# Kernel optimization log

Measured on AMD Instinct MI355X. Metric: run time of the kernel, lower is better.

The kernel has to match this reference:

```python
import jax, jax.numpy as jnp
import numpy as np

D_MODEL = 2048
NUM_HEADS = 16
HEAD_DIM = D_MODEL // NUM_HEADS
EPS = 1e-6


def setup_inputs() -> dict:
    key = jax.random.key(0)
    ks = jax.random.split(key, 5)
    B, S = 1, 4096
    scale = 1.0 / np.sqrt(D_MODEL)
    return {
        "x": jax.random.normal(ks[0], (B, S, D_MODEL), dtype=jnp.float32),
        "wq": jax.random.normal(ks[1], (D_MODEL, D_MODEL), dtype=jnp.float32) * scale,
        "wk": jax.random.normal(ks[2], (D_MODEL, D_MODEL), dtype=jnp.float32) * scale,
        "wv": jax.random.normal(ks[3], (D_MODEL, D_MODEL), dtype=jnp.float32) * scale,
        "wo": jax.random.normal(ks[4], (D_MODEL, D_MODEL), dtype=jnp.float32) * scale,
        "q_norm_w": jnp.ones((HEAD_DIM,), dtype=jnp.float32),
        "k_norm_w": jnp.ones((HEAD_DIM,), dtype=jnp.float32),
    }


def _rmsnorm(x, w):
    rms = jnp.sqrt(jnp.mean(x * x, axis=-1, keepdims=True) + EPS)
    return x / rms * w


def reference(x, wq, wk, wv, wo, q_norm_w, k_norm_w):
    B, S, _ = x.shape
    # nn.Linear: y = x @ W.T ; split heads -> [B, H, S, Dh]
    def proj(w):
        return (x @ w.T).reshape(B, S, NUM_HEADS, HEAD_DIM).transpose(0, 2, 1, 3)
    q = _rmsnorm(proj(wq), q_norm_w)
    k = _rmsnorm(proj(wk), k_norm_w)
    v = proj(wv)
    scale = 1.0 / np.sqrt(HEAD_DIM)
    attn = jnp.einsum("bhqd,bhkd->bhqk", q, k) * scale  # [B,H,S,S]
    attn = jax.nn.softmax(attn, axis=-1)
    out = jnp.einsum("bhqk,bhkd->bhqd", attn, v)
    out = out.transpose(0, 2, 1, 3).reshape(B, S, D_MODEL)
    return out @ wo.T
```

## Files before the change

kernel.cpp:

```cpp
#include <hip/hip_runtime.h>
#include <hip/hip_bf16.h>

#define S 4096
#define D 2048
#define NH 16
#define HD 128

typedef __attribute__((ext_vector_type(8))) short bf16x8;
typedef __attribute__((ext_vector_type(4))) float f32x4;

typedef __attribute__((address_space(1))) char glob_char;
typedef __attribute__((address_space(3))) char lds_char_t;

__device__ __forceinline__ void gld16(const void* g, void* l) {
    __builtin_amdgcn_global_load_lds((const glob_char*)g, (lds_char_t*)l, 16, 0, 0);
}

__device__ __forceinline__ unsigned short f2b(float f) {
    union { float f; unsigned u; } c; c.f = f;
    unsigned r = c.u + 0x7fff + ((c.u >> 16) & 1);
    return (unsigned short)(r >> 16);
}
__device__ __forceinline__ float b2f(unsigned short u) {
    union { unsigned u; float f; } c; c.u = ((unsigned)u) << 16;
    return c.f;
}

__device__ __forceinline__ float fexp2(float x) {
#if __has_builtin(__builtin_amdgcn_exp2f)
    return __builtin_amdgcn_exp2f(x);
#else
    return __expf(x * 0.6931471805599453f);
#endif
}

#define MFMA16(a, b, c) __builtin_amdgcn_mfma_f32_16x16x32_bf16((a), (b), (c), 0, 0, 0)

__global__ __launch_bounds__(256) void cvt_all(
    const float* __restrict__ x,  const float* __restrict__ wq,
    const float* __restrict__ wk, const float* __restrict__ wv,
    const float* __restrict__ wo,
    unsigned short* __restrict__ xb, unsigned short* __restrict__ wqkvb,
    unsigned short* __restrict__ wob)
{
    const int z = blockIdx.y;
    const float* src; unsigned short* dst; int n4;
    if (z == 0)      { src = x;  dst = xb;                        n4 = (S * D) / 4; }
    else if (z == 1) { src = wq; dst = wqkvb;                     n4 = (D * D) / 4; }
    else if (z == 2) { src = wk; dst = wqkvb + (size_t)D * D;     n4 = (D * D) / 4; }
    else if (z == 3) { src = wv; dst = wqkvb + 2 * (size_t)D * D; n4 = (D * D) / 4; }
    else             { src = wo; dst = wob;                       n4 = (D * D) / 4; }
    int i = blockIdx.x * 256 + threadIdx.x;
    if (i < n4) {
        float4 v = ((const float4*)src)[i];
        ushort4 o;
        o.x = f2b(v.x); o.y = f2b(v.y); o.z = f2b(v.z); o.w = f2b(v.w);
        ((ushort4*)dst)[i] = o;
    }
}

__global__ __launch_bounds__(512, 2) void gemm8_qkv(
    const unsigned short* __restrict__ A, const unsigned short* __restrict__ B,
    void* __restrict__ O0, void* __restrict__ O1, void* __restrict__ O2,
    const float* __restrict__ qw, const float* __restrict__ kw)
{
    __shared__ short lds[65536];
    __shared__ float red[4][256];

    const int tid = threadIdx.x;
    const int lane = tid & 63, col = lane & 15, quad = lane >> 4;
    const int w = tid >> 6, wr = w >> 2, wc = w & 3;
    const int m0 = blockIdx.y * 256, n0 = blockIdx.x * 256;

    const int srow = tid >> 3;
    const int sslot = (tid & 7) ^ (srow & 7);
    const unsigned short* pa0 = A + (size_t)(m0 + srow) * 2048 + sslot * 8;
    const unsigned short* pb0 = B + (size_t)(n0 + srow) * 2048 + sslot * 8;
    const int dst0 = tid * 8;

    auto stA = [&](int t, int h, int buf) {
        const unsigned short* g = pa0 + (size_t)h * 262144 + t * 64;
        short* d = &lds[buf * 16384 + h * 8192 + dst0];
        gld16(g, d);
        gld16(g + 131072, d + 4096);
    };
    auto stB = [&](int t, int h, int buf) {
        const unsigned short* g = pb0 + (size_t)h * 262144 + t * 64;
        short* d = &lds[32768 + buf * 16384 + h * 8192 + dst0];
        gld16(g, d);
        gld16(g + 131072, d + 4096);
    };

    const int sl0 = (quad ^ (col & 7)) << 3;
    const int arow = (wr * 128 + col) * 64;
    const int brow = (wc * 64 + col) * 64;
    auto rdA = [&](int mf, int kk, int buf) -> bf16x8 {
        return *(const bf16x8*)&lds[buf * 16384 + arow + mf * 1024 + (sl0 ^ (kk << 5))];
    };
    auto rdB = [&](int nf, int kk, int buf) -> bf16x8 {
        return *(const bf16x8*)&lds[32768 + buf * 16384 + brow + nf * 1024 + (sl0 ^ (kk << 5))];
    };

    f32x4 acc[8][4];
    #pragma unroll
    for (int i = 0; i < 8; ++i)
        #pragma unroll
        for (int j = 0; j < 4; ++j)
            #pragma unroll
            for (int r = 0; r < 4; ++r) acc[i][j][r] = 0.0f;

    stA(0, 0, 0); stA(0, 1, 0); stB(0, 0, 0); stB(0, 1, 0);
    stA(1, 0, 1); stA(1, 1, 1);
    asm volatile("s_waitcnt vmcnt(4)" ::: "memory");
    __builtin_amdgcn_s_barrier();

    for (int t = 0; t < 32; ++t) {
        const int cur = t & 1, nxt = cur ^ 1;
        const bool s1 = t < 31, s2 = t < 30;
        bf16x8 a0[4][2], a1[4][2], b0[2][2], b1[2][2];

        #pragma unroll
        for (int mf = 0; mf < 4; ++mf) { a0[mf][0] = rdA(mf, 0, cur); a0[mf][1] = rdA(mf, 1, cur); }
        #pragma unroll
        for (int nf = 0; nf < 2; ++nf) { b0[nf][0] = rdB(nf, 0, cur); b0[nf][1] = rdB(nf, 1, cur); }
        if (s1) stB(t + 1, 0, nxt);
        __builtin_amdgcn_s_barrier();
        __builtin_amdgcn_s_setprio(1);
        #pragma unroll
        for (int mf = 0; mf < 4; ++mf)
            #pragma unroll
            for (int nf = 0; nf < 2; ++nf) {
                acc[mf][nf] = MFMA16(a0[mf][0], b0[nf][0], acc[mf][nf]);
                acc[mf][nf] = MFMA16(a0[mf][1], b0[nf][1], acc[mf][nf]);
            }
        __builtin_amdgcn_s_setprio(0);
        __builtin_amdgcn_s_barrier();

        #pragma unroll
        for (int mf = 0; mf < 4; ++mf) { a1[mf][0] = rdA(mf + 4, 0, cur); a1[mf][1] = rdA(mf + 4, 1, cur); }
        #pragma unroll
        for (int nf = 0; nf < 2; ++nf) { b1[nf][0] = rdB(nf + 2, 0, cur); b1[nf][1] = rdB(nf + 2, 1, cur); }
        if (s1) stB(t + 1, 1, nxt);
        __builtin_amdgcn_s_barrier();
        __builtin_amdgcn_s_setprio(1);
        #pragma unroll
        for (int mf = 0; mf < 4; ++mf)
            #pragma unroll
            for (int nf = 0; nf < 2; ++nf) {
                acc[mf][nf + 2] = MFMA16(a0[mf][0], b1[nf][0], acc[mf][nf + 2]);
                acc[mf][nf + 2] = MFMA16(a0[mf][1], b1[nf][1], acc[mf][nf + 2]);
            }
        __builtin_amdgcn_s_setprio(0);
        __builtin_amdgcn_s_barrier();

        if (s2) stA(t + 2, 0, cur);
        __builtin_amdgcn_s_barrier();
        __builtin_amdgcn_s_setprio(1);
        #pragma unroll
        for (int mf = 0; mf < 4; ++mf)
            #pragma unroll
            for (int nf = 0; nf < 2; ++nf) {
                acc[mf + 4][nf] = MFMA16(a1[mf][0], b0[nf][0], acc[mf + 4][nf]);
                acc[mf + 4][nf] = MFMA16(a1[mf][1], b0[nf][1], acc[mf + 4][nf]);
            }
        __builtin_amdgcn_s_setprio(0);
        __builtin_amdgcn_s_barrier();

        if (s2) stA(t + 2, 1, cur);
        __builtin_amdgcn_s_barrier();
        __builtin_amdgcn_s_setprio(1);
        #pragma unroll
        for (int mf = 0; mf < 4; ++mf)
            #pragma unroll
            for (int nf = 0; nf < 2; ++nf) {
                acc[mf + 4][nf + 2] = MFMA16(a1[mf][0], b1[nf][0], acc[mf + 4][nf + 2]);
                acc[mf + 4][nf + 2] = MFMA16(a1[mf][1], b1[nf][1], acc[mf + 4][nf + 2]);
            }
        __builtin_amdgcn_s_setprio(0);
        if (s2)      asm volatile("s_waitcnt vmcnt(4)" ::: "memory");
        else if (s1) asm volatile("s_waitcnt vmcnt(0)" ::: "memory");
        __builtin_amdgcn_s_barrier();
    }

    const int sel = n0 >> 11;
    if (sel == 2) {
        unsigned short* VtO = (unsigned short*)O2;
        #pragma unroll
        for (int mf = 0; mf < 8; ++mf)
            #pragma unroll
            for (int nf = 0; nf < 4; ++nf) {
                int n = (n0 & 2047) + wc * 64 + nf * 16 + col;
                int hh = n >> 7, dv = n & 127;
                ushort4 pk;
                pk.x = f2b(acc[mf][nf][0]); pk.y = f2b(acc[mf][nf][1]);
                pk.z = f2b(acc[mf][nf][2]); pk.w = f2b(acc[mf][nf][3]);
                *(ushort4*)&VtO[(size_t)hh * (HD * S) + (size_t)dv * S +
                                m0 + wr * 128 + mf * 16 + quad * 4] = pk;
            }
    } else {
        unsigned short* C = (unsigned short*)(sel == 0 ? O0 : O1);
        const float* wgt = (sel == 0) ? qw : kw;
        const float extra = (sel == 0)
            ? 0.08838834764831845f * 1.4426950408889634f : 1.0f;
        float wv4[4];
        #pragma unroll
        for (int nf = 0; nf < 4; ++nf)
            wv4[nf] = wgt[(wc & 1) * 64 + nf * 16 + col];
        #pragma unroll
        for (int mf = 0; mf < 8; ++mf)
            #pragma unroll
            for (int r = 0; r < 4; ++r) {
                float ss = 0.0f;
                #pragma unroll
                for (int nf = 0; nf < 4; ++nf) ss += acc[mf][nf][r] * acc[mf][nf][r];
                #pragma unroll
                for (int d = 1; d < 16; d <<= 1) ss += __shfl_xor(ss, d, 64);
                if (col == 0) red[wc][wr * 128 + mf * 16 + quad * 4 + r] = ss;
            }
        __syncthreads();
        #pragma unroll
        for (int mf = 0; mf < 8; ++mf) {
            float rsc[4];
            #pragma unroll
            for (int r = 0; r < 4; ++r) {
                int idx = wr * 128 + mf * 16 + quad * 4 + r;
                float tot = red[wc & 6][idx] + red[(wc & 6) + 1][idx];
                rsc[r] = rsqrtf(tot * (1.0f / HD) + 1e-6f) * extra;
            }
            #pragma unroll
            for (int nf = 0; nf < 4; ++nf)
                #pragma unroll
                for (int r = 0; r < 4; ++r)
                    C[(size_t)(m0 + wr * 128 + mf * 16 + quad * 4 + r) * 2048 +
                      (n0 & 2047) + wc * 64 + nf * 16 + col] =
                        f2b(acc[mf][nf][r] * rsc[r] * wv4[nf]);
        }
    }
}

__global__ __launch_bounds__(256) void gemm_out(
    const unsigned short* __restrict__ A, const unsigned short* __restrict__ B,
    float* __restrict__ C)
{
    __shared__ short As[128 * 32];
    __shared__ short Bs[128 * 32];

    const int tid = threadIdx.x;
    const int m0 = blockIdx.y * 128, n0 = blockIdx.x * 128;
    const int w = tid >> 6, lane = tid & 63, col = lane & 15, quad = lane >> 4;
    const int mw = (w >> 1) * 64, nw = (w & 1) * 64;

    const int r0 = tid >> 2, k80 = (tid & 3) << 3;
    const size_t aoff = (size_t)(m0 + r0) * 2048 + k80;
    const size_t boff = (size_t)(n0 + r0) * 2048 + k80;

    f32x4 acc[4][4];
    #pragma unroll
    for (int i = 0; i < 4; ++i)
        #pragma unroll
        for (int j = 0; j < 4; ++j)
            #pragma unroll
            for (int r = 0; r < 4; ++r) acc[i][j][r] = 0.0f;

    for (int k0 = 0; k0 < 2048; k0 += 32) {
        gld16(&A[aoff + k0],               &As[tid * 8]);
        gld16(&A[aoff + 64 * 2048 + k0],   &As[(tid + 256) * 8]);
        gld16(&B[boff + k0],               &Bs[tid * 8]);
        gld16(&B[boff + 64 * 2048 + k0],   &Bs[(tid + 256) * 8]);
        __syncthreads();
        bf16x8 af[4], bf[4];
        #pragma unroll
        for (int i = 0; i < 4; ++i)
            af[i] = *(const bf16x8*)&As[(mw + 16 * i + col) * 32 + quad * 8];
        #pragma unroll
        for (int j = 0; j < 4; ++j)
            bf[j] = *(const bf16x8*)&Bs[(nw + 16 * j + col) * 32 + quad * 8];
        #pragma unroll
        for (int i = 0; i < 4; ++i)
            #pragma unroll
            for (int j = 0; j < 4; ++j)
                acc[i][j] = MFMA16(af[i], bf[j], acc[i][j]);
        __syncthreads();
    }

    #pragma unroll
    for (int i = 0; i < 4; ++i)
        #pragma unroll
        for (int j = 0; j < 4; ++j)
            #pragma unroll
            for (int r = 0; r < 4; ++r)
                C[(size_t)(m0 + mw + 16 * i + quad * 4 + r) * 2048 + n0 + nw + 16 * j + col] = acc[i][j][r];
}

struct FlashSmem {
    short Ks[2][8192];
    short Vs[2][8192];
    short Ps[8192];
};

__global__ __launch_bounds__(256, 2) void flash_mfma(
    const unsigned short* __restrict__ Qg, const unsigned short* __restrict__ Kg,
    const unsigned short* __restrict__ Vt, unsigned short* __restrict__ Ctx)
{
    __shared__ FlashSmem sm;

    const int tid = threadIdx.x;
    const int w = tid >> 6, lane = tid & 63, col = lane & 15, quad = lane >> 4;
    const int q0 = blockIdx.x * 128, h = blockIdx.y;

    bf16x8 aq[2][4];
    #pragma unroll
    for (int qs = 0; qs < 2; ++qs) {
        const size_t qoff = (size_t)(q0 + w * 32 + qs * 16 + col) * 2048 + h * 128 + quad * 8;
        #pragma unroll
        for (int ds = 0; ds < 4; ++ds)
            aq[qs][ds] = *(const bf16x8*)&Qg[qoff + ds * 32];
    }

    const unsigned short* kga[4];
    const unsigned short* vga[4];
    #pragma unroll
    for (int it = 0; it < 4; ++it) {
        int c = tid + (it << 8);
        {   int ds = c >> 8, rem = c & 255, key = rem >> 2, ch = rem & 3;
            int g = ch ^ ((key >> 1) & 3);
            kga[it] = &Kg[(size_t)key * 2048 + h * 128 + ds * 32 + g * 8]; }
        {   int ks = c >> 9, rem = c & 511, dv = rem >> 2, ch = rem & 3;
            int g = ch ^ ((dv >> 1) & 3);
            vga[it] = &Vt[(size_t)h * (HD * S) + (size_t)dv * S + ks * 32 + g * 8]; }
    }

    const int fb = col * 32 + ((quad ^ ((col >> 1) & 3)) << 3);
    int ap_off[2][2];
    #pragma unroll
    for (int qs = 0; qs < 2; ++qs) {
        int qrow = w * 32 + qs * 16 + col;
        #pragma unroll
        for (int ks = 0; ks < 2; ++ks) {
            int k0 = ks * 32 + quad * 8;
            ap_off[ks][qs] = qrow * 64 + (k0 ^ ((qrow & 7) << 3));
        }
    }
    int psb2[2][4];
    #pragma unroll
    for (int qs = 0; qs < 2; ++qs)
        #pragma unroll
        for (int r = 0; r < 4; ++r) {
            int ql = w * 32 + qs * 16 + quad * 4 + r;
            int s = (ql & 7) << 3;
            psb2[qs][r] = ql * 64 + (col ^ (s & 8)) + (s & 48);
        }

    bf16x8 vone;
    #pragma unroll
    for (int i = 0; i < 8; ++i) vone[i] = (short)0x3F80;

    f32x4 lacc[2];
    f32x4 o[2][8];
    #pragma unroll
    for (int qs = 0; qs < 2; ++qs) {
        #pragma unroll
        for (int r = 0; r < 4; ++r) lacc[qs][r] = 0.0f;
        #pragma unroll
        for (int nj = 0; nj < 8; ++nj)
            #pragma unroll
            for (int r = 0; r < 4; ++r) o[qs][nj][r] = 0.0f;
    }

    auto stage = [&](int b) {
        #pragma unroll
        for (int it = 0; it < 4; ++it) {
            gld16(kga[it], &sm.Ks[b][(tid + (it << 8)) * 8]);
            kga[it] += 64 * 2048;
        }
        #pragma unroll
        for (int it = 0; it < 4; ++it) {
            gld16(vga[it], &sm.Vs[b][(tid + (it << 8)) * 8]);
            vga[it] += 64;
        }
    };

    auto compute = [&](int b) {
        f32x4 sc[2][4];
        #pragma unroll
        for (int qs = 0; qs < 2; ++qs)
            #pragma unroll
            for (int kj = 0; kj < 4; ++kj)
                #pragma unroll
                for (int r = 0; r < 4; ++r) sc[qs][kj][r] = 0.0f;
        __builtin_amdgcn_s_setprio(1);
        #pragma unroll
        for (int ds = 0; ds < 4; ++ds)
            #pragma unroll
            for (int kj = 0; kj < 4; ++kj) {
                bf16x8 bk = *(const bf16x8*)&sm.Ks[b][fb + ds * 2048 + kj * 512];
                sc[0][kj] = MFMA16(aq[0][ds], bk, sc[0][kj]);
                sc[1][kj] = MFMA16(aq[1][ds], bk, sc[1][kj]);
            }
        __builtin_amdgcn_s_setprio(0);

        #pragma unroll
        for (int qs = 0; qs < 2; ++qs)
            #pragma unroll
            for (int kj = 0; kj < 4; ++kj)
                #pragma unroll
                for (int r = 0; r < 4; ++r)
                    sm.Ps[psb2[qs][r] ^ (kj * 16)] = (short)f2b(fexp2(sc[qs][kj][r]));

        __builtin_amdgcn_s_setprio(1);
        #pragma unroll
        for (int ks = 0; ks < 2; ++ks) {
            bf16x8 ap0 = *(const bf16x8*)&sm.Ps[ap_off[ks][0]];
            bf16x8 ap1 = *(const bf16x8*)&sm.Ps[ap_off[ks][1]];
            lacc[0] = MFMA16(ap0, vone, lacc[0]);
            lacc[1] = MFMA16(ap1, vone, lacc[1]);
            #pragma unroll
            for (int nj = 0; nj < 8; ++nj) {
                bf16x8 bv = *(const bf16x8*)&sm.Vs[b][fb + ks * 4096 + nj * 512];
                o[0][nj] = MFMA16(ap0, bv, o[0][nj]);
                o[1][nj] = MFMA16(ap1, bv, o[1][nj]);
            }
        }
        __builtin_amdgcn_s_setprio(0);
    };

    stage(0);
    for (int j0 = 0; j0 < S; j0 += 128) {
        __syncthreads();
        stage(1);
        compute(0);
        __syncthreads();
        if (j0 + 128 < S) stage(0);
        compute(1);
    }

    #pragma unroll
    for (int qs = 0; qs < 2; ++qs) {
        float inv[4];
        #pragma unroll
        for (int r = 0; r < 4; ++r) inv[r] = 1.0f / lacc[qs][r];
        #pragma unroll
        for (int nj = 0; nj < 8; ++nj)
            #pragma unroll
            for (int r = 0; r < 4; ++r)
                Ctx[(size_t)(q0 + w * 32 + qs * 16 + quad * 4 + r) * 2048 + h * 128 + nj * 16 + col] =
                    f2b(o[qs][nj][r] * inv[r]);
    }
}

extern "C" void kernel_launch(void* const* d_in, const int* in_sizes, int n_in,
                              void* d_out, int out_size, void* d_ws, size_t ws_size,
                              hipStream_t stream)
{
    const float* x  = (const float*)d_in[0];
    const float* wq = (const float*)d_in[1];
    const float* wk = (const float*)d_in[2];
    const float* wv = (const float*)d_in[3];
    const float* wo = (const float*)d_in[4];
    const float* qw = (const float*)d_in[5];
    const float* kw = (const float*)d_in[6];
    float* out = (float*)d_out;

    const size_t MB = 1u << 20;
    char* ws = (char*)d_ws;
    unsigned short* xb    = (unsigned short*)(ws);
    unsigned short* Wqkvb = (unsigned short*)(ws + 16 * MB);
    unsigned short* Wob   = (unsigned short*)(ws + 40 * MB);
    unsigned short* Qb    = (unsigned short*)(ws + 48 * MB);
    unsigned short* Kb    = (unsigned short*)(ws + 64 * MB);
    unsigned short* Vt    = (unsigned short*)(ws + 80 * MB);
    unsigned short* Ctx   = xb;

    cvt_all<<<dim3(8192, 5), dim3(256), 0, stream>>>(x, wq, wk, wv, wo, xb, Wqkvb, Wob);

    gemm8_qkv<<<dim3(24, 16), dim3(512), 0, stream>>>(xb, Wqkvb, Qb, Kb, Vt, qw, kw);

    flash_mfma<<<dim3(32, 16), dim3(256), 0, stream>>>(Qb, Kb, Vt, Ctx);

    gemm_out<<<dim3(16, 32), dim3(256), 0, stream>>>(Ctx, Wob, out);
}
```

Before: 451.6 us.

## Load V fragments directly from global into registers instead of staging in LDS

Removes the double-buffered V tile from shared memory and instead has each lane load its V^T B-operand fragments straight from global memory into registers at the start of each compute step. This frees LDS (which could raise occupancy) and removes the V async-copy traffic. The cost is that every wave redundantly fetches the same V data from global/L2, with exposed load latency and no prefetch overlap, plus higher register pressure from 16 bf16x8 fragments.

```diff
diff --git a/kernel.cpp b/kernel.cpp
--- a/kernel.cpp
+++ b/kernel.cpp
@@ -20,10 +20,6 @@
     union { float f; unsigned u; } c; c.f = f;
     unsigned r = c.u + 0x7fff + ((c.u >> 16) & 1);
     return (unsigned short)(r >> 16);
-}
-__device__ __forceinline__ float b2f(unsigned short u) {
-    union { unsigned u; float f; } c; c.u = ((unsigned)u) << 16;
-    return c.f;
 }
 
 __device__ __forceinline__ float fexp2(float x) {
@@ -294,7 +290,6 @@
 
 struct FlashSmem {
     short Ks[2][8192];
-    short Vs[2][8192];
     short Ps[8192];
 };
 
@@ -318,17 +313,14 @@
     }
 
     const unsigned short* kga[4];
-    const unsigned short* vga[4];
     #pragma unroll
     for (int it = 0; it < 4; ++it) {
         int c = tid + (it << 8);
-        {   int ds = c >> 8, rem = c & 255, key = rem >> 2, ch = rem & 3;
-            int g = ch ^ ((key >> 1) & 3);
-            kga[it] = &Kg[(size_t)key * 2048 + h * 128 + ds * 32 + g * 8]; }
-        {   int ks = c >> 9, rem = c & 511, dv = rem >> 2, ch = rem & 3;
-            int g = ch ^ ((dv >> 1) & 3);
-            vga[it] = &Vt[(size_t)h * (HD * S) + (size_t)dv * S + ks * 32 + g * 8]; }
-    }
+        int ds = c >> 8, rem = c & 255, key = rem >> 2, ch = rem & 3;
+        int g = ch ^ ((key >> 1) & 3);
+        kga[it] = &Kg[(size_t)key * 2048 + h * 128 + ds * 32 + g * 8];
+    }
+    const unsigned short* vrow = Vt + (size_t)h * (HD * S) + (size_t)col * S + quad * 8;
 
     const int fb = col * 32 + ((quad ^ ((col >> 1) & 3)) << 3);
     int ap_off[2][2];
@@ -373,14 +365,16 @@
             gld16(kga[it], &sm.Ks[b][(tid + (it << 8)) * 8]);
             kga[it] += 64 * 2048;
         }
-        #pragma unroll
-        for (int it = 0; it < 4; ++it) {
-            gld16(vga[it], &sm.Vs[b][(tid + (it << 8)) * 8]);
-            vga[it] += 64;
-        }
-    };
-
-    auto compute = [&](int b) {
+    };
+
+    auto compute = [&](int b, int kk0) {
+        bf16x8 bv[2][8];
+        #pragma unroll
+        for (int ks = 0; ks < 2; ++ks)
+            #pragma unroll
+            for (int nj = 0; nj < 8; ++nj)
+                bv[ks][nj] = *(const bf16x8*)&vrow[(size_t)nj * (16 * S) + ks * 32 + kk0];
+
         f32x4 sc[2][4];
         #pragma unroll
         for (int qs = 0; qs < 2; ++qs)
@@ -416,9 +410,8 @@
             lacc[1] = MFMA16(ap1, vone, lacc[1]);
             #pragma unroll
             for (int nj = 0; nj < 8; ++nj) {
-                bf16x8 bv = *(const bf16x8*)&sm.Vs[b][fb + ks * 4096 + nj * 512];
-                o[0][nj] = MFMA16(ap0, bv, o[0][nj]);
-                o[1][nj] = MFMA16(ap1, bv, o[1][nj]);
+                o[0][nj] = MFMA16(ap0, bv[ks][nj], o[0][nj]);
+                o[1][nj] = MFMA16(ap1, bv[ks][nj], o[1][nj]);
             }
         }
         __builtin_amdgcn_s_setprio(0);
@@ -428,10 +421,10 @@
     for (int j0 = 0; j0 < S; j0 += 128) {
         __syncthreads();
         stage(1);
-        compute(0);
+        compute(0, j0);
         __syncthreads();
         if (j0 + 128 < S) stage(0);
-        compute(1);
+        compute(1, j0 + 64);
     }
 
     #pragma unroll
```

Result: slower. 579.7 us (+28.4%).
